# Optimization experiments

Measured on AMD Instinct MI355X. Metric: run time of the kernel, lower is better.

## Reference

```python
import jax, jax.numpy as jnp
import numpy as np

N_NODES = 50000
N_EDGES = 1200000
H = 64
N_CONV = 3
N_GRAPHS = 64
N_CLASSES = 10


def rbf_cutoff(d):
    # Gaussian radial basis over (0,1) with cosine cutoff, per edge -> [E, H]
    mu = jnp.linspace(0.0, 1.0, H, dtype=d.dtype)
    gamma = jnp.asarray(float(H), d.dtype)  # inverse width
    bf = jnp.exp(-gamma * (d[:, None] - mu[None, :]) ** 2)
    cut = 0.5 * (jnp.cos(jnp.pi * jnp.clip(d, 0.0, 1.0)) + 1.0)
    return bf * cut[:, None]


def mlp(x, W1, b1, W2, b2):
    # Linear -> softplus -> Linear (SchNet-style filter/embedding MLP)
    return jax.nn.softplus(x @ W1 + b1) @ W2 + b2


def setup_inputs() -> dict:
    key = jax.random.key(0)
    ks = jax.random.split(key, 12)
    s = 0.1  # weight scale for numerical stability
    inp = {
        "d": jax.random.uniform(ks[0], (N_EDGES,), jnp.float32),
        "W_emb1": s * jax.random.normal(ks[1], (H, H), jnp.float32),
        "b_emb1": jnp.zeros((H,), jnp.float32),
        "W_emb2": s * jax.random.normal(ks[2], (H, H), jnp.float32),
        "b_emb2": jnp.zeros((H,), jnp.float32),
        "filt_W1": s * jax.random.normal(ks[3], (N_CONV, H, H), jnp.float32),
        "filt_b1": jnp.zeros((N_CONV, H), jnp.float32),
        "filt_W2": s * jax.random.normal(ks[4], (N_CONV, H, H), jnp.float32),
        "filt_b2": jnp.zeros((N_CONV, H), jnp.float32),
        "W_in": s * jax.random.normal(ks[5], (N_CONV, H, H), jnp.float32),
        "b_in": jnp.zeros((N_CONV, H), jnp.float32),
        "W_out": s * jax.random.normal(ks[6], (N_CONV, H, H), jnp.float32),
        "b_out": jnp.zeros((N_CONV, H), jnp.float32),
        "W_fc": s * jax.random.normal(ks[7], (H, N_CLASSES), jnp.float32),
        "b_fc": jnp.zeros((N_CLASSES,), jnp.float32),
        "src": jax.random.randint(ks[8], (N_EDGES,), 0, N_NODES, jnp.int32),
        "dst": jax.random.randint(ks[9], (N_EDGES,), 0, N_NODES, jnp.int32),
        "node_graph_ids": jnp.sort(jax.random.randint(ks[10], (N_NODES,), 0, N_GRAPHS, jnp.int32)),
    }
    return inp


def reference(d, W_emb1, b_emb1, W_emb2, b_emb2,
              filt_W1, filt_b1, filt_W2, filt_b2,
              W_in, b_in, W_out, b_out, W_fc, b_fc,
              src, dst, node_graph_ids):
    bf = rbf_cutoff(d)  # [E, H], basis * cutoff (g.edata['bf'])

    # SchnetEmbedding: MLP over radial features, scatter-add to destination nodes
    x = jax.ops.segment_sum(mlp(bf, W_emb1, b_emb1, W_emb2, b_emb2),
                            dst, num_segments=N_NODES)  # [N, H]

    # Stacked SchnetConv: gather x[src] -> in-proj -> radial filter modulation -> scatter-add -> out-proj
    for l in range(N_CONV):
        filt = mlp(bf, filt_W1[l], filt_b1[l], filt_W2[l], filt_b2[l])  # [E, H]
        m = (x[src] @ W_in[l] + b_in[l]) * filt                          # [E, H]
        agg = jax.ops.segment_sum(m, dst, num_segments=N_NODES)         # [N, H]
        x = jax.nn.relu(agg @ W_out[l] + b_out[l])

    # dgl.mean_nodes: per-graph mean pooling
    counts = jax.ops.segment_sum(jnp.ones((N_NODES,), x.dtype),
                                 node_graph_ids, num_segments=N_GRAPHS)
    pooled = jax.ops.segment_sum(x, node_graph_ids, num_segments=N_GRAPHS)
    pooled = pooled / jnp.maximum(counts, 1.0)[:, None]  # [B, H]

    logits = pooled @ W_fc + b_fc
    return jax.nn.log_softmax(logits, axis=1)
```

## Files before the change

kernel.cpp:

```cpp
#include <hip/hip_runtime.h>
#include <math.h>

#define H 64
#define NCONV 3
#define NGRAPHS 64
#define NCLASSES 10
#define TBL 8192
#define TROWS (TBL + 1)
#define CAP 6144
#define EPT 8

typedef unsigned short bfu;

__device__ __forceinline__ float bf2f(bfu u) {
    return __uint_as_float(((unsigned int)u) << 16);
}
__device__ __forceinline__ bfu f2bf(float f) {
    unsigned int x = __float_as_uint(f);
    return (bfu)((x + 0x7FFF + ((x >> 16) & 1)) >> 16);
}
__device__ __forceinline__ float softplus_f(float x) {
    return fmaxf(x, 0.f) + log1pf(expf(-fabsf(x)));
}
__device__ __forceinline__ float bflo(unsigned int u) { return __uint_as_float(u << 16); }
__device__ __forceinline__ float bfhi(unsigned int u) { return __uint_as_float(u & 0xFFFF0000u); }

__device__ __forceinline__ unsigned int ld_rec_nt(const unsigned int* p) {
    return __builtin_nontemporal_load(p);
}
#define REC_SRC(u) ((u) & 0x1FFFFu)
#define REC_T(u)   ((u) >> 17)

__global__ void build_tables(const float* __restrict__ W_emb1, const float* __restrict__ b_emb1,
                             const float* __restrict__ W_emb2, const float* __restrict__ b_emb2,
                             const float* __restrict__ fW1, const float* __restrict__ fb1,
                             const float* __restrict__ fW2, const float* __restrict__ fb2,
                             bfu* __restrict__ tabs)
{
    int which = blockIdx.y;
    const float *W1, *b1, *W2, *b2;
    if (which == 0) { W1 = W_emb1; b1 = b_emb1; W2 = W_emb2; b2 = b_emb2; }
    else {
        int l = which - 1;
        W1 = fW1 + l * H * H; b1 = fb1 + l * H;
        W2 = fW2 + l * H * H; b2 = fb2 + l * H;
    }

    __shared__ float sW1[H * H], sW2[H * H];
    __shared__ float sb1[H], sb2[H];
    __shared__ float sha[4][H], shb[4][H];

    int tid = threadIdx.x;
    for (int i = tid; i < H * H; i += 256) { sW1[i] = W1[i]; sW2[i] = W2[i]; }
    if (tid < H) sb1[tid] = b1[tid];
    else if (tid < 2 * H) sb2[tid - H] = b2[tid - H];
    __syncthreads();

    int wave = tid >> 6, lane = tid & 63;
    int base = blockIdx.x * 64;
    int lim  = min(base + 64, TROWS);

    for (int r = base + wave; r < lim; r += 4) {
        float dv   = (float)r / (float)TBL;
        float mu   = (float)lane / (float)(H - 1);
        float diff = dv - mu;
        float cut  = 0.5f * (cosf(3.14159265358979323846f * dv) + 1.0f);
        float bfj  = expf(-(float)H * diff * diff) * cut;

        sha[wave][lane] = bfj;
        float a = sb1[lane];
        #pragma unroll
        for (int i = 0; i < H; ++i) a = fmaf(sha[wave][i], sW1[i * H + lane], a);
        shb[wave][lane] = softplus_f(a);
        float a2 = sb2[lane];
        #pragma unroll
        for (int i = 0; i < H; ++i) a2 = fmaf(shb[wave][i], sW2[i * H + lane], a2);

        tabs[((size_t)which * TROWS + r) * H + lane] = f2bf(a2);
    }
}

__global__ void coarse_part(const int* __restrict__ src, const int* __restrict__ dst,
                            const float* __restrict__ d, int* __restrict__ ccur,
                            unsigned long long* __restrict__ cbuf, int E, int ncb)
{
    __shared__ int lcnt[256];
    __shared__ int lbase[256];
    int tid = threadIdx.x;
    int e0  = blockIdx.x * (256 * EPT);

    lcnt[tid] = 0;
    __syncthreads();

    int mybin[EPT], myrank[EPT];
    unsigned long long myrec[EPT];
    #pragma unroll
    for (int k = 0; k < EPT; ++k) {
        int e = e0 + k * 256 + tid;
        mybin[k] = -1;
        if (e < E) {
            int v = dst[e];
            int bin = v >> 8;
            float dv = fminf(fmaxf(d[e], 0.f), 1.f);
            int t = (int)(dv * (float)TBL + 0.5f);
            t = min(t, TBL);
            unsigned int p31 = (unsigned int)src[e] | ((unsigned int)t << 17);
            myrec[k]  = (unsigned long long)p31 | ((unsigned long long)(v & 255) << 32);
            mybin[k]  = bin;
            myrank[k] = atomicAdd(&lcnt[bin], 1);
        }
    }
    __syncthreads();

    {
        int c = (tid < ncb) ? lcnt[tid] : 0;
        lbase[tid] = (c > 0) ? atomicAdd(&ccur[tid], c) : 0;
    }
    __syncthreads();

    #pragma unroll
    for (int k = 0; k < EPT; ++k) {
        if (mybin[k] >= 0) {
            cbuf[(size_t)mybin[k] * CAP + lbase[mybin[k]] + myrank[k]] = myrec[k];
        }
    }
}

__global__ void cscan(const int* __restrict__ ccur, int* __restrict__ cstart,
                      int* __restrict__ off, int E, int N, int ncb)
{
    __shared__ int s[256];
    int t = threadIdx.x;
    int v = (t < ncb) ? ccur[t] : 0;
    s[t] = v;
    __syncthreads();
    for (int o = 1; o < 256; o <<= 1) {
        int u = (t >= o) ? s[t - o] : 0;
        __syncthreads();
        s[t] += u;
        __syncthreads();
    }
    if (t < ncb) cstart[t] = s[t] - v;
    if (t == 0) off[N] = E;
}

__global__ void fine_sort(const unsigned long long* __restrict__ cbuf,
                          const int* __restrict__ ccur, const int* __restrict__ cstart,
                          int* __restrict__ off, unsigned int* __restrict__ recs, int N)
{
    __shared__ int lcnt[256];
    __shared__ int ss[256];
    __shared__ int lcur[256];
    int bin  = blockIdx.x;
    int tid  = threadIdx.x;
    int cnt  = ccur[bin];
    int base = cstart[bin];
    const unsigned long long* buf = cbuf + (size_t)bin * CAP;

    lcnt[tid] = 0;
    __syncthreads();
    for (int i = tid; i < cnt; i += 256) {
        int j = (int)((buf[i] >> 32) & 255);
        atomicAdd(&lcnt[j], 1);
    }
    __syncthreads();
    int v = lcnt[tid];
    ss[tid] = v;
    __syncthreads();
    for (int o = 1; o < 256; o <<= 1) {
        int u = (tid >= o) ? ss[tid - o] : 0;
        __syncthreads();
        ss[tid] += u;
        __syncthreads();
    }
    int excl = ss[tid] - v;
    lcur[tid] = excl;
    int node = bin * 256 + tid;
    if (node < N) off[node] = base + excl;
    __syncthreads();
    for (int i = tid; i < cnt; i += 256) {
        unsigned long long r = buf[i];
        int j = (int)((r >> 32) & 255);
        int pos = base + atomicAdd(&lcur[j], 1);
        recs[pos] = (unsigned int)(r & 0x7FFFFFFFu);
    }
}

__global__ void emb_fused(const int* __restrict__ off, const unsigned int* __restrict__ recs,
                          const bfu* __restrict__ tab, const float* __restrict__ W,
                          const float* __restrict__ bvec, bfu* __restrict__ yout, int N)
{
    __shared__ float sW[H * H];
    __shared__ float sb[H];
    __shared__ float sx[4][H];
    int tid = threadIdx.x;
    for (int i = tid; i < H * H; i += 256) sW[i] = W[i];
    if (tid < H) sb[tid] = bvec[tid];
    __syncthreads();

    const unsigned int* tab32 = (const unsigned int*)tab;

    int wave = tid >> 6, lane = tid & 63;
    int half = lane >> 5;
    int li   = lane & 31;

    for (int k = 0; k < 4; ++k) {
        int node = blockIdx.x * 16 + k * 4 + wave;
        if (node >= N) continue;
        int b = off[node], en = off[node + 1];
        int deg = en - b;
        int c0  = (deg + 1) >> 1;
        int p   = b + half * c0;
        int e   = (half == 0) ? (b + c0) : en;

        float a0 = 0.f, a1 = 0.f, a2 = 0.f, a3 = 0.f;

        if (e - p >= 8) {
            unsigned int u0 = ld_rec_nt(recs + p);
            unsigned int u1 = ld_rec_nt(recs + p + 1);
            unsigned int u2 = ld_rec_nt(recs + p + 2);
            unsigned int u3 = ld_rec_nt(recs + p + 3);
            unsigned int tv0 = tab32[(size_t)REC_T(u0) * 32 + li];
            unsigned int tv1 = tab32[(size_t)REC_T(u1) * 32 + li];
            unsigned int tv2 = tab32[(size_t)REC_T(u2) * 32 + li];
            unsigned int tv3 = tab32[(size_t)REC_T(u3) * 32 + li];
            u0 = ld_rec_nt(recs + p + 4);
            u1 = ld_rec_nt(recs + p + 5);
            u2 = ld_rec_nt(recs + p + 6);
            u3 = ld_rec_nt(recs + p + 7);
            while (p + 12 <= e) {
                unsigned int w0 = ld_rec_nt(recs + p + 8);
                unsigned int w1 = ld_rec_nt(recs + p + 9);
                unsigned int w2 = ld_rec_nt(recs + p + 10);
                unsigned int w3 = ld_rec_nt(recs + p + 11);
                unsigned int n0 = tab32[(size_t)REC_T(u0) * 32 + li];
                unsigned int n1 = tab32[(size_t)REC_T(u1) * 32 + li];
                unsigned int n2 = tab32[(size_t)REC_T(u2) * 32 + li];
                unsigned int n3 = tab32[(size_t)REC_T(u3) * 32 + li];
                a0 += bflo(tv0); a1 += bfhi(tv0);
                a2 += bflo(tv1); a3 += bfhi(tv1);
                a0 += bflo(tv2); a1 += bfhi(tv2);
                a2 += bflo(tv3); a3 += bfhi(tv3);
                tv0 = n0; tv1 = n1; tv2 = n2; tv3 = n3;
                u0 = w0; u1 = w1; u2 = w2; u3 = w3;
                p += 4;
            }
            unsigned int n0 = tab32[(size_t)REC_T(u0) * 32 + li];
            unsigned int n1 = tab32[(size_t)REC_T(u1) * 32 + li];
            unsigned int n2 = tab32[(size_t)REC_T(u2) * 32 + li];
            unsigned int n3 = tab32[(size_t)REC_T(u3) * 32 + li];
            a0 += bflo(tv0); a1 += bfhi(tv0);
            a2 += bflo(tv1); a3 += bfhi(tv1);
            a0 += bflo(tv2); a1 += bfhi(tv2);
            a2 += bflo(tv3); a3 += bfhi(tv3);
            a0 += bflo(n0); a1 += bfhi(n0);
            a2 += bflo(n1); a3 += bfhi(n1);
            a0 += bflo(n2); a1 += bfhi(n2);
            a2 += bflo(n3); a3 += bfhi(n3);
            p += 8;
        } else if (e - p >= 4) {
            unsigned int u0 = ld_rec_nt(recs + p);
            unsigned int u1 = ld_rec_nt(recs + p + 1);
            unsigned int u2 = ld_rec_nt(recs + p + 2);
            unsigned int u3 = ld_rec_nt(recs + p + 3);
            unsigned int n0 = tab32[(size_t)REC_T(u0) * 32 + li];
            unsigned int n1 = tab32[(size_t)REC_T(u1) * 32 + li];
            unsigned int n2 = tab32[(size_t)REC_T(u2) * 32 + li];
            unsigned int n3 = tab32[(size_t)REC_T(u3) * 32 + li];
            a0 += bflo(n0); a1 += bfhi(n0);
            a2 += bflo(n1); a3 += bfhi(n1);
            a0 += bflo(n2); a1 += bfhi(n2);
            a2 += bflo(n3); a3 += bfhi(n3);
            p += 4;
        }
        for (; p < e; ++p) {
            unsigned int u = ld_rec_nt(recs + p);
            unsigned int t = tab32[(size_t)REC_T(u) * 32 + li];
            a0 += bflo(t); a1 += bfhi(t);
        }

        float alo = a0 + a2, ahi = a1 + a3;
        alo += __shfl_down(alo, 32);
        ahi += __shfl_down(ahi, 32);
        if (lane < 32) {
            sx[wave][2 * li]     = alo;
            sx[wave][2 * li + 1] = ahi;
        }
        float o = sb[lane];
        #pragma unroll
        for (int i = 0; i < H; ++i) o = fmaf(sx[wave][i], sW[i * H + lane], o);
        yout[(size_t)node * H + lane] = f2bf(o);
    }
}

template <bool LAST>
__global__ void conv_fused_k(const int* __restrict__ off, const unsigned int* __restrict__ recs,
                             const bfu* __restrict__ tab, const bfu* __restrict__ y,
                             const float* __restrict__ W_out, const float* __restrict__ b_out,
                             const float* __restrict__ W_in, const float* __restrict__ b_in,
                             bfu* __restrict__ yout, float* __restrict__ xout, int N)
{
    __shared__ unsigned int sWo[H * H / 2];
    __shared__ unsigned int sWi[H * H / 2];
    __shared__ float sbo[H], sbi[H];
    __shared__ float sx[4][H];
    int tid = threadIdx.x;
    for (int i = tid; i < H * H / 2; i += 256) {
        int i2 = i >> 6, l = i & 63;
        sWo[i] = (unsigned int)f2bf(W_out[(2 * i2) * H + l]) |
                 ((unsigned int)f2bf(W_out[(2 * i2 + 1) * H + l]) << 16);
        if (!LAST)
            sWi[i] = (unsigned int)f2bf(W_in[(2 * i2) * H + l]) |
                     ((unsigned int)f2bf(W_in[(2 * i2 + 1) * H + l]) << 16);
    }
    if (tid < H) sbo[tid] = b_out[tid];
    else if (!LAST && tid < 2 * H) sbi[tid - H] = b_in[tid - H];
    __syncthreads();

    const unsigned int* tab32 = (const unsigned int*)tab;
    const unsigned int* y32   = (const unsigned int*)y;

    int wave = tid >> 6, lane = tid & 63;
    int half = lane >> 5;
    int li   = lane & 31;

    for (int k = 0; k < 4; ++k) {
        int node = blockIdx.x * 16 + k * 4 + wave;
        if (node >= N) continue;
        int b = off[node], en = off[node + 1];
        int deg = en - b;
        int c0  = (deg + 1) >> 1;
        int p   = b + half * c0;
        int e   = (half == 0) ? (b + c0) : en;

        float a0 = 0.f, a1 = 0.f, a2 = 0.f, a3 = 0.f;

        if (e - p >= 8) {
            unsigned int u0 = ld_rec_nt(recs + p);
            unsigned int u1 = ld_rec_nt(recs + p + 1);
            unsigned int u2 = ld_rec_nt(recs + p + 2);
            unsigned int u3 = ld_rec_nt(recs + p + 3);
            unsigned int tv0 = tab32[(size_t)REC_T(u0) * 32 + li];
            unsigned int yv0 = y32[(size_t)REC_SRC(u0) * 32 + li];
            unsigned int tv1 = tab32[(size_t)REC_T(u1) * 32 + li];
            unsigned int yv1 = y32[(size_t)REC_SRC(u1) * 32 + li];
            unsigned int tv2 = tab32[(size_t)REC_T(u2) * 32 + li];
            unsigned int yv2 = y32[(size_t)REC_SRC(u2) * 32 + li];
            unsigned int tv3 = tab32[(size_t)REC_T(u3) * 32 + li];
            unsigned int yv3 = y32[(size_t)REC_SRC(u3) * 32 + li];
            u0 = ld_rec_nt(recs + p + 4);
            u1 = ld_rec_nt(recs + p + 5);
            u2 = ld_rec_nt(recs + p + 6);
            u3 = ld_rec_nt(recs + p + 7);
            while (p + 12 <= e) {
                unsigned int w0 = ld_rec_nt(recs + p + 8);
                unsigned int w1 = ld_rec_nt(recs + p + 9);
                unsigned int w2 = ld_rec_nt(recs + p + 10);
                unsigned int w3 = ld_rec_nt(recs + p + 11);
                unsigned int nt0 = tab32[(size_t)REC_T(u0) * 32 + li];
                unsigned int ny0 = y32[(size_t)REC_SRC(u0) * 32 + li];
                unsigned int nt1 = tab32[(size_t)REC_T(u1) * 32 + li];
                unsigned int ny1 = y32[(size_t)REC_SRC(u1) * 32 + li];
                unsigned int nt2 = tab32[(size_t)REC_T(u2) * 32 + li];
                unsigned int ny2 = y32[(size_t)REC_SRC(u2) * 32 + li];
                unsigned int nt3 = tab32[(size_t)REC_T(u3) * 32 + li];
                unsigned int ny3 = y32[(size_t)REC_SRC(u3) * 32 + li];
                a0 = fmaf(bflo(yv0), bflo(tv0), a0);
                a1 = fmaf(bfhi(yv0), bfhi(tv0), a1);
                a2 = fmaf(bflo(yv1), bflo(tv1), a2);
                a3 = fmaf(bfhi(yv1), bfhi(tv1), a3);
                a0 = fmaf(bflo(yv2), bflo(tv2), a0);
                a1 = fmaf(bfhi(yv2), bfhi(tv2), a1);
                a2 = fmaf(bflo(yv3), bflo(tv3), a2);
                a3 = fmaf(bfhi(yv3), bfhi(tv3), a3);
                tv0 = nt0; yv0 = ny0; tv1 = nt1; yv1 = ny1;
                tv2 = nt2; yv2 = ny2; tv3 = nt3; yv3 = ny3;
                u0 = w0; u1 = w1; u2 = w2; u3 = w3;
                p += 4;
            }
            unsigned int nt0 = tab32[(size_t)REC_T(u0) * 32 + li];
            unsigned int ny0 = y32[(size_t)REC_SRC(u0) * 32 + li];
            unsigned int nt1 = tab32[(size_t)REC_T(u1) * 32 + li];
            unsigned int ny1 = y32[(size_t)REC_SRC(u1) * 32 + li];
            unsigned int nt2 = tab32[(size_t)REC_T(u2) * 32 + li];
            unsigned int ny2 = y32[(size_t)REC_SRC(u2) * 32 + li];
            unsigned int nt3 = tab32[(size_t)REC_T(u3) * 32 + li];
            unsigned int ny3 = y32[(size_t)REC_SRC(u3) * 32 + li];
            a0 = fmaf(bflo(yv0), bflo(tv0), a0);
            a1 = fmaf(bfhi(yv0), bfhi(tv0), a1);
            a2 = fmaf(bflo(yv1), bflo(tv1), a2);
            a3 = fmaf(bfhi(yv1), bfhi(tv1), a3);
            a0 = fmaf(bflo(yv2), bflo(tv2), a0);
            a1 = fmaf(bfhi(yv2), bfhi(tv2), a1);
            a2 = fmaf(bflo(yv3), bflo(tv3), a2);
            a3 = fmaf(bfhi(yv3), bfhi(tv3), a3);
            a0 = fmaf(bflo(ny0), bflo(nt0), a0);
            a1 = fmaf(bfhi(ny0), bfhi(nt0), a1);
            a2 = fmaf(bflo(ny1), bflo(nt1), a2);
            a3 = fmaf(bfhi(ny1), bfhi(nt1), a3);
            a0 = fmaf(bflo(ny2), bflo(nt2), a0);
            a1 = fmaf(bfhi(ny2), bfhi(nt2), a1);
            a2 = fmaf(bflo(ny3), bflo(nt3), a2);
            a3 = fmaf(bfhi(ny3), bfhi(nt3), a3);
            p += 8;
        } else if (e - p >= 4) {
            unsigned int u0 = ld_rec_nt(recs + p);
            unsigned int u1 = ld_rec_nt(recs + p + 1);
            unsigned int u2 = ld_rec_nt(recs + p + 2);
            unsigned int u3 = ld_rec_nt(recs + p + 3);
            unsigned int nt0 = tab32[(size_t)REC_T(u0) * 32 + li];
            unsigned int ny0 = y32[(size_t)REC_SRC(u0) * 32 + li];
            unsigned int nt1 = tab32[(size_t)REC_T(u1) * 32 + li];
            unsigned int ny1 = y32[(size_t)REC_SRC(u1) * 32 + li];
            unsigned int nt2 = tab32[(size_t)REC_T(u2) * 32 + li];
            unsigned int ny2 = y32[(size_t)REC_SRC(u2) * 32 + li];
            unsigned int nt3 = tab32[(size_t)REC_T(u3) * 32 + li];
            unsigned int ny3 = y32[(size_t)REC_SRC(u3) * 32 + li];
            a0 = fmaf(bflo(ny0), bflo(nt0), a0);
            a1 = fmaf(bfhi(ny0), bfhi(nt0), a1);
            a2 = fmaf(bflo(ny1), bflo(nt1), a2);
            a3 = fmaf(bfhi(ny1), bfhi(nt1), a3);
            a0 = fmaf(bflo(ny2), bflo(nt2), a0);
            a1 = fmaf(bfhi(ny2), bfhi(nt2), a1);
            a2 = fmaf(bflo(ny3), bflo(nt3), a2);
            a3 = fmaf(bfhi(ny3), bfhi(nt3), a3);
            p += 4;
        }
        for (; p < e; ++p) {
            unsigned int u = ld_rec_nt(recs + p);
            unsigned int t = tab32[(size_t)REC_T(u) * 32 + li];
            unsigned int v = y32[(size_t)REC_SRC(u) * 32 + li];
            a0 = fmaf(bflo(v), bflo(t), a0);
            a1 = fmaf(bfhi(v), bfhi(t), a1);
        }

        float alo = a0 + a2, ahi = a1 + a3;
        alo += __shfl_down(alo, 32);
        ahi += __shfl_down(ahi, 32);
        if (lane < 32) {
            sx[wave][2 * li]     = alo;
            sx[wave][2 * li + 1] = ahi;
        }
        float o = sbo[lane];
        #pragma unroll
        for (int i2 = 0; i2 < H / 2; ++i2) {
            unsigned int u = sWo[i2 * H + lane];
            o = fmaf(sx[wave][2 * i2],     bflo(u), o);
            o = fmaf(sx[wave][2 * i2 + 1], bfhi(u), o);
        }
        o = fmaxf(o, 0.f);
        if (LAST) {
            xout[(size_t)node * H + lane] = o;
        } else {
            sx[wave][lane] = o;
            float o2 = sbi[lane];
            #pragma unroll
            for (int i2 = 0; i2 < H / 2; ++i2) {
                unsigned int u = sWi[i2 * H + lane];
                o2 = fmaf(sx[wave][2 * i2],     bflo(u), o2);
                o2 = fmaf(sx[wave][2 * i2 + 1], bfhi(u), o2);
            }
            yout[(size_t)node * H + lane] = f2bf(o2);
        }
    }
}

__global__ void pool_kernel(const float* __restrict__ x, const int* __restrict__ gid,
                            float* __restrict__ pooled, float* __restrict__ counts, int N)
{
    int wavesPerBlock = blockDim.x >> 6;
    int wid  = blockIdx.x * wavesPerBlock + (threadIdx.x >> 6);
    int lane = threadIdx.x & 63;
    int totalWaves = gridDim.x * wavesPerBlock;
    int chunk = (N + totalWaves - 1) / totalWaves;
    int beg = wid * chunk, end = min(beg + chunk, N);
    if (beg >= end) return;

    float acc = 0.f;
    int cur = -1, cnt = 0;
    for (int n = beg; n < end; ++n) {
        int g = gid[n];
        if (g != cur) {
            if (cur >= 0) {
                atomicAdd(&pooled[(size_t)cur * H + lane], acc);
                if (lane == 0) atomicAdd(&counts[cur], (float)cnt);
            }
            cur = g; acc = 0.f; cnt = 0;
        }
        acc += x[(size_t)n * H + lane];
        cnt++;
    }
    atomicAdd(&pooled[(size_t)cur * H + lane], acc);
    if (lane == 0) atomicAdd(&counts[cur], (float)cnt);
}

__global__ void head_kernel(const float* __restrict__ pooled, const float* __restrict__ counts,
                            const float* __restrict__ Wfc, const float* __restrict__ bfc,
                            float* __restrict__ out)
{
    int g = blockIdx.x;
    int c = threadIdx.x;
    __shared__ float logits[NCLASSES];
    float cnt = fmaxf(counts[g], 1.0f);
    if (c < NCLASSES) {
        float acc = bfc[c];
        #pragma unroll
        for (int i = 0; i < H; ++i)
            acc = fmaf(pooled[(size_t)g * H + i] / cnt, Wfc[i * NCLASSES + c], acc);
        logits[c] = acc;
    }
    __syncthreads();
    if (c < NCLASSES) {
        float m = -INFINITY;
        #pragma unroll
        for (int k = 0; k < NCLASSES; ++k) m = fmaxf(m, logits[k]);
        float s = 0.f;
        #pragma unroll
        for (int k = 0; k < NCLASSES; ++k) s += expf(logits[k] - m);
        out[g * NCLASSES + c] = logits[c] - m - logf(s);
    }
}

extern "C" void kernel_launch(void* const* d_in, const int* in_sizes, int n_in,
                              void* d_out, int out_size, void* d_ws, size_t ws_size,
                              hipStream_t stream)
{
    const float* d_d    = (const float*)d_in[0];
    const float* W_emb1 = (const float*)d_in[1];
    const float* b_emb1 = (const float*)d_in[2];
    const float* W_emb2 = (const float*)d_in[3];
    const float* b_emb2 = (const float*)d_in[4];
    const float* fW1    = (const float*)d_in[5];
    const float* fb1    = (const float*)d_in[6];
    const float* fW2    = (const float*)d_in[7];
    const float* fb2    = (const float*)d_in[8];
    const float* W_in   = (const float*)d_in[9];
    const float* b_in   = (const float*)d_in[10];
    const float* W_out  = (const float*)d_in[11];
    const float* b_out  = (const float*)d_in[12];
    const float* W_fc   = (const float*)d_in[13];
    const float* b_fc   = (const float*)d_in[14];
    const int*   src    = (const int*)d_in[15];
    const int*   dst    = (const int*)d_in[16];
    const int*   gid    = (const int*)d_in[17];

    const int E = in_sizes[0];
    const int N = in_sizes[17];
    const int ncb = (N + 255) >> 8;

    float* out = (float*)d_out;

    char* base = (char*)d_ws;
    unsigned int* recs = (unsigned int*)base;   base += (size_t)E * 4;
    bfu*  tabs   = (bfu*)base;                  base += (size_t)4 * TROWS * H * 2;
    bfu*  yA     = (bfu*)base;                  base += (size_t)N * H * 2;
    bfu*  yB     = (bfu*)base;                  base += (size_t)N * H * 2;
    size_t usz   = (size_t)N * H * 4;
    size_t csz   = (size_t)ncb * CAP * 8;
    char* uni    = base;                        base += (usz > csz ? usz : csz);
    float* x3    = (float*)uni;
    unsigned long long* cbuf = (unsigned long long*)uni;
    float* pooled= (float*)base;                base += (size_t)NGRAPHS * H * 4;
    float* counts= (float*)base;                base += (size_t)NGRAPHS * 4;
    int*  off    = (int*)base;                  base += (size_t)(N + 1) * 4;
    int*  ccur   = (int*)base;                  base += 256 * 4;
    int*  cstart = (int*)base;                  base += 256 * 4;

    const int node_blocks16 = (N + 15) / 16;
    const int part_blocks   = (E + 256 * EPT - 1) / (256 * EPT);

    dim3 tg((TROWS + 63) / 64, 4);
    build_tables<<<tg, 256, 0, stream>>>(W_emb1, b_emb1, W_emb2, b_emb2,
                                         fW1, fb1, fW2, fb2, tabs);

    hipMemsetAsync(ccur, 0, 256 * 4, stream);
    coarse_part<<<part_blocks, 256, 0, stream>>>(src, dst, d_d, ccur, cbuf, E, ncb);
    cscan<<<1, 256, 0, stream>>>(ccur, cstart, off, E, N, ncb);
    fine_sort<<<ncb, 256, 0, stream>>>(cbuf, ccur, cstart, off, recs, N);

    emb_fused<<<node_blocks16, 256, 0, stream>>>(off, recs, tabs, W_in, b_in, yA, N);

    conv_fused_k<false><<<node_blocks16, 256, 0, stream>>>(
        off, recs, tabs + (size_t)1 * TROWS * H, yA,
        W_out, b_out, W_in + (size_t)1 * H * H, b_in + (size_t)1 * H, yB, nullptr, N);
    conv_fused_k<false><<<node_blocks16, 256, 0, stream>>>(
        off, recs, tabs + (size_t)2 * TROWS * H, yB,
        W_out + (size_t)1 * H * H, b_out + (size_t)1 * H,
        W_in + (size_t)2 * H * H, b_in + (size_t)2 * H, yA, nullptr, N);
    conv_fused_k<true><<<node_blocks16, 256, 0, stream>>>(
        off, recs, tabs + (size_t)3 * TROWS * H, yA,
        W_out + (size_t)2 * H * H, b_out + (size_t)2 * H,
        nullptr, nullptr, nullptr, x3, N);

    hipMemsetAsync(pooled, 0, ((size_t)NGRAPHS * H + NGRAPHS) * 4, stream);
    pool_kernel<<<128, 256, 0, stream>>>(x3, gid, pooled, counts, N);

    head_kernel<<<NGRAPHS, 64, 0, stream>>>(pooled, counts, W_fc, b_fc, out);
}
```

Before: 321.6 us.

## Gather rows with 16-lane uint2 loads, four edges per wave in flight

Reworks the per-node gather in the embedding and conv kernels. Each wave is now split into four 16-lane groups, and each group reads a 64-wide bf16 row with 8-byte uint2 loads. Before, it was two 32-lane halves using 4-byte loads. Four edges are processed per step and the partial sums are reduced with xor shuffles, aiming for wider memory transactions and fewer load instructions per edge. The trade-offs are a shallower software pipeline (one record ahead per group instead of four) and an extra shuffle stage.

Measured after the change: 334.6 us. +4.0%, slower.

```diff
diff --git a/kernel.cpp b/kernel.cpp
--- a/kernel.cpp
+++ b/kernel.cpp
@@ -198,93 +198,63 @@
     if (tid < H) sb[tid] = bvec[tid];
     __syncthreads();
 
-    const unsigned int* tab32 = (const unsigned int*)tab;
+    const uint2* tab2 = (const uint2*)tab;
 
     int wave = tid >> 6, lane = tid & 63;
-    int half = lane >> 5;
-    int li   = lane & 31;
+    int q  = lane >> 4;
+    int li = lane & 15;
 
     for (int k = 0; k < 4; ++k) {
         int node = blockIdx.x * 16 + k * 4 + wave;
         if (node >= N) continue;
         int b = off[node], en = off[node + 1];
-        int deg = en - b;
-        int c0  = (deg + 1) >> 1;
-        int p   = b + half * c0;
-        int e   = (half == 0) ? (b + c0) : en;
+        int deg   = en - b;
+        int nfull = deg >> 2;
 
         float a0 = 0.f, a1 = 0.f, a2 = 0.f, a3 = 0.f;
-
-        if (e - p >= 8) {
+        int p = b + q;
+
+        if (nfull >= 2) {
             unsigned int u0 = ld_rec_nt(recs + p);
-            unsigned int u1 = ld_rec_nt(recs + p + 1);
-            unsigned int u2 = ld_rec_nt(recs + p + 2);
-            unsigned int u3 = ld_rec_nt(recs + p + 3);
-            unsigned int tv0 = tab32[(size_t)REC_T(u0) * 32 + li];
-            unsigned int tv1 = tab32[(size_t)REC_T(u1) * 32 + li];
-            unsigned int tv2 = tab32[(size_t)REC_T(u2) * 32 + li];
-            unsigned int tv3 = tab32[(size_t)REC_T(u3) * 32 + li];
-            u0 = ld_rec_nt(recs + p + 4);
-            u1 = ld_rec_nt(recs + p + 5);
-            u2 = ld_rec_nt(recs + p + 6);
-            u3 = ld_rec_nt(recs + p + 7);
-            while (p + 12 <= e) {
-                unsigned int w0 = ld_rec_nt(recs + p + 8);
-                unsigned int w1 = ld_rec_nt(recs + p + 9);
-                unsigned int w2 = ld_rec_nt(recs + p + 10);
-                unsigned int w3 = ld_rec_nt(recs + p + 11);
-                unsigned int n0 = tab32[(size_t)REC_T(u0) * 32 + li];
-                unsigned int n1 = tab32[(size_t)REC_T(u1) * 32 + li];
-                unsigned int n2 = tab32[(size_t)REC_T(u2) * 32 + li];
-                unsigned int n3 = tab32[(size_t)REC_T(u3) * 32 + li];
-                a0 += bflo(tv0); a1 += bfhi(tv0);
-                a2 += bflo(tv1); a3 += bfhi(tv1);
-                a0 += bflo(tv2); a1 += bfhi(tv2);
-                a2 += bflo(tv3); a3 += bfhi(tv3);
-                tv0 = n0; tv1 = n1; tv2 = n2; tv3 = n3;
-                u0 = w0; u1 = w1; u2 = w2; u3 = w3;
+            unsigned int u1 = ld_rec_nt(recs + p + 4);
+            p += 8;
+            uint2 tv0 = tab2[(size_t)REC_T(u0) * 16 + li];
+            for (int it = 2; it < nfull; ++it) {
+                unsigned int u2 = ld_rec_nt(recs + p);
                 p += 4;
+                uint2 tv1 = tab2[(size_t)REC_T(u1) * 16 + li];
+                a0 += bflo(tv0.x); a1 += bfhi(tv0.x);
+                a2 += bflo(tv0.y); a3 += bfhi(tv0.y);
+                u1 = u2; tv0 = tv1;
             }
-            unsigned int n0 = tab32[(size_t)REC_T(u0) * 32 + li];
-            unsigned int n1 = tab32[(size_t)REC_T(u1) * 32 + li];
-            unsigned int n2 = tab32[(size_t)REC_T(u2) * 32 + li];
-            unsigned int n3 = tab32[(size_t)REC_T(u3) * 32 + li];
-            a0 += bflo(tv0); a1 += bfhi(tv0);
-            a2 += bflo(tv1); a3 += bfhi(tv1);
-            a0 += bflo(tv2); a1 += bfhi(tv2);
-            a2 += bflo(tv3); a3 += bfhi(tv3);
-            a0 += bflo(n0); a1 += bfhi(n0);
-            a2 += bflo(n1); a3 += bfhi(n1);
-            a0 += bflo(n2); a1 += bfhi(n2);
-            a2 += bflo(n3); a3 += bfhi(n3);
-            p += 8;
-        } else if (e - p >= 4) {
+            uint2 tv1 = tab2[(size_t)REC_T(u1) * 16 + li];
+            a0 += bflo(tv0.x); a1 += bfhi(tv0.x);
+            a2 += bflo(tv0.y); a3 += bfhi(tv0.y);
+            a0 += bflo(tv1.x); a1 += bfhi(tv1.x);
+            a2 += bflo(tv1.y); a3 += bfhi(tv1.y);
+        } else if (nfull == 1) {
             unsigned int u0 = ld_rec_nt(recs + p);
-            unsigned int u1 = ld_rec_nt(recs + p + 1);
-            unsigned int u2 = ld_rec_nt(recs + p + 2);
-            unsigned int u3 = ld_rec_nt(recs + p + 3);
-            unsigned int n0 = tab32[(size_t)REC_T(u0) * 32 + li];
-            unsigned int n1 = tab32[(size_t)REC_T(u1) * 32 + li];
-            unsigned int n2 = tab32[(size_t)REC_T(u2) * 32 + li];
-            unsigned int n3 = tab32[(size_t)REC_T(u3) * 32 + li];
-            a0 += bflo(n0); a1 += bfhi(n0);
-            a2 += bflo(n1); a3 += bfhi(n1);
-            a0 += bflo(n2); a1 += bfhi(n2);
-            a2 += bflo(n3); a3 += bfhi(n3);
-            p += 4;
-        }
-        for (; p < e; ++p) {
-            unsigned int u = ld_rec_nt(recs + p);
-            unsigned int t = tab32[(size_t)REC_T(u) * 32 + li];
-            a0 += bflo(t); a1 += bfhi(t);
-        }
-
-        float alo = a0 + a2, ahi = a1 + a3;
-        alo += __shfl_down(alo, 32);
-        ahi += __shfl_down(ahi, 32);
-        if (lane < 32) {
-            sx[wave][2 * li]     = alo;
-            sx[wave][2 * li + 1] = ahi;
+            uint2 tv0 = tab2[(size_t)REC_T(u0) * 16 + li];
+            a0 += bflo(tv0.x); a1 += bfhi(tv0.x);
+            a2 += bflo(tv0.y); a3 += bfhi(tv0.y);
+        }
+        int r = deg & 3;
+        if (q < r) {
+            unsigned int u = ld_rec_nt(recs + b + 4 * nfull + q);
+            uint2 tv = tab2[(size_t)REC_T(u) * 16 + li];
+            a0 += bflo(tv.x); a1 += bfhi(tv.x);
+            a2 += bflo(tv.y); a3 += bfhi(tv.y);
+        }
+
+        a0 += __shfl_xor(a0, 16); a0 += __shfl_xor(a0, 32);
+        a1 += __shfl_xor(a1, 16); a1 += __shfl_xor(a1, 32);
+        a2 += __shfl_xor(a2, 16); a2 += __shfl_xor(a2, 32);
+        a3 += __shfl_xor(a3, 16); a3 += __shfl_xor(a3, 32);
+        if (lane < 16) {
+            sx[wave][4 * li + 0] = a0;
+            sx[wave][4 * li + 1] = a1;
+            sx[wave][4 * li + 2] = a2;
+            sx[wave][4 * li + 3] = a3;
         }
         float o = sb[lane];
         #pragma unroll
@@ -317,129 +287,79 @@
     else if (!LAST && tid < 2 * H) sbi[tid - H] = b_in[tid - H];
     __syncthreads();
 
-    const unsigned int* tab32 = (const unsigned int*)tab;
-    const unsigned int* y32   = (const unsigned int*)y;
+    const uint2* tab2 = (const uint2*)tab;
+    const uint2* y2   = (const uint2*)y;
 
     int wave = tid >> 6, lane = tid & 63;
-    int half = lane >> 5;
-    int li   = lane & 31;
+    int q  = lane >> 4;
+    int li = lane & 15;
 
     for (int k = 0; k < 4; ++k) {
         int node = blockIdx.x * 16 + k * 4 + wave;
         if (node >= N) continue;
         int b = off[node], en = off[node + 1];
-        int deg = en - b;
-        int c0  = (deg + 1) >> 1;
-        int p   = b + half * c0;
-        int e   = (half == 0) ? (b + c0) : en;
+        int deg   = en - b;
+        int nfull = deg >> 2;
 
         float a0 = 0.f, a1 = 0.f, a2 = 0.f, a3 = 0.f;
-
-        if (e - p >= 8) {
+        int p = b + q;
+
+        if (nfull >= 2) {
             unsigned int u0 = ld_rec_nt(recs + p);
-            unsigned int u1 = ld_rec_nt(recs + p + 1);
-            unsigned int u2 = ld_rec_nt(recs + p + 2);
-            unsigned int u3 = ld_rec_nt(recs + p + 3);
-            unsigned int tv0 = tab32[(size_t)REC_T(u0) * 32 + li];
-            unsigned int yv0 = y32[(size_t)REC_SRC(u0) * 32 + li];
-            unsigned int tv1 = tab32[(size_t)REC_T(u1) * 32 + li];
-            unsigned int yv1 = y32[(size_t)REC_SRC(u1) * 32 + li];
-            unsigned int tv2 = tab32[(size_t)REC_T(u2) * 32 + li];
-            unsigned int yv2 = y32[(size_t)REC_SRC(u2) * 32 + li];
-            unsigned int tv3 = tab32[(size_t)REC_T(u3) * 32 + li];
-            unsigned int yv3 = y32[(size_t)REC_SRC(u3) * 32 + li];
-            u0 = ld_rec_nt(recs + p + 4);
-            u1 = ld_rec_nt(recs + p + 5);
-            u2 = ld_rec_nt(recs + p + 6);
-            u3 = ld_rec_nt(recs + p + 7);
-            while (p + 12 <= e) {
-                unsigned int w0 = ld_rec_nt(recs + p + 8);
-                unsigned int w1 = ld_rec_nt(recs + p + 9);
-                unsigned int w2 = ld_rec_nt(recs + p + 10);
-                unsigned int w3 = ld_rec_nt(recs + p + 11);
-                unsigned int nt0 = tab32[(size_t)REC_T(u0) * 32 + li];
-                unsigned int ny0 = y32[(size_t)REC_SRC(u0) * 32 + li];
-                unsigned int nt1 = tab32[(size_t)REC_T(u1) * 32 + li];
-                unsigned int ny1 = y32[(size_t)REC_SRC(u1) * 32 + li];
-                unsigned int nt2 = tab32[(size_t)REC_T(u2) * 32 + li];
-                unsigned int ny2 = y32[(size_t)REC_SRC(u2) * 32 + li];
-                unsigned int nt3 = tab32[(size_t)REC_T(u3) * 32 + li];
-                unsigned int ny3 = y32[(size_t)REC_SRC(u3) * 32 + li];
-                a0 = fmaf(bflo(yv0), bflo(tv0), a0);
-                a1 = fmaf(bfhi(yv0), bfhi(tv0), a1);
-                a2 = fmaf(bflo(yv1), bflo(tv1), a2);
-                a3 = fmaf(bfhi(yv1), bfhi(tv1), a3);
-                a0 = fmaf(bflo(yv2), bflo(tv2), a0);
-                a1 = fmaf(bfhi(yv2), bfhi(tv2), a1);
-                a2 = fmaf(bflo(yv3), bflo(tv3), a2);
-                a3 = fmaf(bfhi(yv3), bfhi(tv3), a3);
-                tv0 = nt0; yv0 = ny0; tv1 = nt1; yv1 = ny1;
-                tv2 = nt2; yv2 = ny2; tv3 = nt3; yv3 = ny3;
-                u0 = w0; u1 = w1; u2 = w2; u3 = w3;
+            unsigned int u1 = ld_rec_nt(recs + p + 4);
+            p += 8;
+            uint2 tv0 = tab2[(size_t)REC_T(u0) * 16 + li];
+            uint2 yv0 = y2[(size_t)REC_SRC(u0) * 16 + li];
+            for (int it = 2; it < nfull; ++it) {
+                unsigned int u2 = ld_rec_nt(recs + p);
                 p += 4;
+                uint2 tv1 = tab2[(size_t)REC_T(u1) * 16 + li];
+                uint2 yv1 = y2[(size_t)REC_SRC(u1) * 16 + li];
+                a0 = fmaf(bflo(yv0.x), bflo(tv0.x), a0);
+                a1 = fmaf(bfhi(yv0.x), bfhi(tv0.x), a1);
+                a2 = fmaf(bflo(yv0.y), bflo(tv0.y), a2);
+                a3 = fmaf(bfhi(yv0.y), bfhi(tv0.y), a3);
+                u1 = u2; tv0 = tv1; yv0 = yv1;
             }
-            unsigned int nt0 = tab32[(size_t)REC_T(u0) * 32 + li];
-            unsigned int ny0 = y32[(size_t)REC_SRC(u0) * 32 + li];
-            unsigned int nt1 = tab32[(size_t)REC_T(u1) * 32 + li];
-            unsigned int ny1 = y32[(size_t)REC_SRC(u1) * 32 + li];
-            unsigned int nt2 = tab32[(size_t)REC_T(u2) * 32 + li];
-            unsigned int ny2 = y32[(size_t)REC_SRC(u2) * 32 + li];
-            unsigned int nt3 = tab32[(size_t)REC_T(u3) * 32 + li];
-            unsigned int ny3 = y32[(size_t)REC_SRC(u3) * 32 + li];
-            a0 = fmaf(bflo(yv0), bflo(tv0), a0);
-            a1 = fmaf(bfhi(yv0), bfhi(tv0), a1);
-            a2 = fmaf(bflo(yv1), bflo(tv1), a2);
-            a3 = fmaf(bfhi(yv1), bfhi(tv1), a3);
-            a0 = fmaf(bflo(yv2), bflo(tv2), a0);
-            a1 = fmaf(bfhi(yv2), bfhi(tv2), a1);
-            a2 = fmaf(bflo(yv3), bflo(tv3), a2);
-            a3 = fmaf(bfhi(yv3), bfhi(tv3), a3);
-            a0 = fmaf(bflo(ny0), bflo(nt0), a0);
-            a1 = fmaf(bfhi(ny0), bfhi(nt0), a1);
-            a2 = fmaf(bflo(ny1), bflo(nt1), a2);
-            a3 = fmaf(bfhi(ny1), bfhi(nt1), a3);
-            a0 = fmaf(bflo(ny2), bflo(nt2), a0);
-            a1 = fmaf(bfhi(ny2), bfhi(nt2), a1);
-            a2 = fmaf(bflo(ny3), bflo(nt3), a2);
-            a3 = fmaf(bfhi(ny3), bfhi(nt3), a3);
-            p += 8;
-        } else if (e - p >= 4) {
+            uint2 tv1 = tab2[(size_t)REC_T(u1) * 16 + li];
+            uint2 yv1 = y2[(size_t)REC_SRC(u1) * 16 + li];
+            a0 = fmaf(bflo(yv0.x), bflo(tv0.x), a0);
+            a1 = fmaf(bfhi(yv0.x), bfhi(tv0.x), a1);
+            a2 = fmaf(bflo(yv0.y), bflo(tv0.y), a2);
+            a3 = fmaf(bfhi(yv0.y), bfhi(tv0.y), a3);
+            a0 = fmaf(bflo(yv1.x), bflo(tv1.x), a0);
+            a1 = fmaf(bfhi(yv1.x), bfhi(tv1.x), a1);
+            a2 = fmaf(bflo(yv1.y), bflo(tv1.y), a2);
+            a3 = fmaf(bfhi(yv1.y), bfhi(tv1.y), a3);
+        } else if (nfull == 1) {
             unsigned int u0 = ld_rec_nt(recs + p);
-            unsigned int u1 = ld_rec_nt(recs + p + 1);
-            unsigned int u2 = ld_rec_nt(recs + p + 2);
-            unsigned int u3 = ld_rec_nt(recs + p + 3);
-            unsigned int nt0 = tab32[(size_t)REC_T(u0) * 32 + li];
-            unsigned int ny0 = y32[(size_t)REC_SRC(u0) * 32 + li];
-            unsigned int nt1 = tab32[(size_t)REC_T(u1) * 32 + li];
-            unsigned int ny1 = y32[(size_t)REC_SRC(u1) * 32 + li];
-            unsigned int nt2 = tab32[(size_t)REC_T(u2) * 32 + li];
-            unsigned int ny2 = y32[(size_t)REC_SRC(u2) * 32 + li];
-            unsigned int nt3 = tab32[(size_t)REC_T(u3) * 32 + li];
-            unsigned int ny3 = y32[(size_t)REC_SRC(u3) * 32 + li];
-            a0 = fmaf(bflo(ny0), bflo(nt0), a0);
-            a1 = fmaf(bfhi(ny0), bfhi(nt0), a1);
-            a2 = fmaf(bflo(ny1), bflo(nt1), a2);
-            a3 = fmaf(bfhi(ny1), bfhi(nt1), a3);
-            a0 = fmaf(bflo(ny2), bflo(nt2), a0);
-            a1 = fmaf(bfhi(ny2), bfhi(nt2), a1);
-            a2 = fmaf(bflo(ny3), bflo(nt3), a2);
-            a3 = fmaf(bfhi(ny3), bfhi(nt3), a3);
-            p += 4;
-        }
-        for (; p < e; ++p) {
-            unsigned int u = ld_rec_nt(recs + p);
-            unsigned int t = tab32[(size_t)REC_T(u) * 32 + li];
-            unsigned int v = y32[(size_t)REC_SRC(u) * 32 + li];
-            a0 = fmaf(bflo(v), bflo(t), a0);
-            a1 = fmaf(bfhi(v), bfhi(t), a1);
-        }
-
-        float alo = a0 + a2, ahi = a1 + a3;
-        alo += __shfl_down(alo, 32);
-        ahi += __shfl_down(ahi, 32);
-        if (lane < 32) {
-            sx[wave][2 * li]     = alo;
-            sx[wave][2 * li + 1] = ahi;
+            uint2 tv0 = tab2[(size_t)REC_T(u0) * 16 + li];
+            uint2 yv0 = y2[(size_t)REC_SRC(u0) * 16 + li];
+            a0 = fmaf(bflo(yv0.x), bflo(tv0.x), a0);
+            a1 = fmaf(bfhi(yv0.x), bfhi(tv0.x), a1);
+            a2 = fmaf(bflo(yv0.y), bflo(tv0.y), a2);
+            a3 = fmaf(bfhi(yv0.y), bfhi(tv0.y), a3);
+        }
+        int r = deg & 3;
+        if (q < r) {
+            unsigned int u = ld_rec_nt(recs + b + 4 * nfull + q);
+            uint2 tv = tab2[(size_t)REC_T(u) * 16 + li];
+            uint2 yv = y2[(size_t)REC_SRC(u) * 16 + li];
+            a0 = fmaf(bflo(yv.x), bflo(tv.x), a0);
+            a1 = fmaf(bfhi(yv.x), bfhi(tv.x), a1);
+            a2 = fmaf(bflo(yv.y), bflo(tv.y), a2);
+            a3 = fmaf(bfhi(yv.y), bfhi(tv.y), a3);
+        }
+
+        a0 += __shfl_xor(a0, 16); a0 += __shfl_xor(a0, 32);
+        a1 += __shfl_xor(a1, 16); a1 += __shfl_xor(a1, 32);
+        a2 += __shfl_xor(a2, 16); a2 += __shfl_xor(a2, 32);
+        a3 += __shfl_xor(a3, 16); a3 += __shfl_xor(a3, 32);
+        if (lane < 16) {
+            sx[wave][4 * li + 0] = a0;
+            sx[wave][4 * li + 1] = a1;
+            sx[wave][4 * li + 2] = a2;
+            sx[wave][4 * li + 3] = a3;
         }
         float o = sbo[lane];
         #pragma unroll
```
